# Kernel tuning notes

Hardware: AMD Instinct MI355X
Metric: run time of the kernel (lower is better)

Reference implementation:

```python
import jax, jax.numpy as jnp
import numpy as np

N = 10000          # nodes
DEG = 16           # incoming edges per node
E = N * DEG
D_IN = 2048        # backbone embed dim
RED = 4
D = D_IN // RED    # 512, gnn embed dim
NHEAD = 8
HD = D // NHEAD    # 64
DHID = 4 * D       # 2048, mlp hidden
L = 2              # num gnn layers
NCLS = 751
EPS = 1e-5


def _layernorm(x, g, b):
    m = jnp.mean(x, axis=-1, keepdims=True)
    v = jnp.var(x, axis=-1, keepdims=True)
    return (x - m) * jax.lax.rsqrt(v + EPS) * g + b


def _attention_layer(feats, r, c, Wq, bq, Wk, bk, Wv, bv, Wo, bo,
                     g1, be1, W1, b1, W2, b2, g2, be2):
    # MultiHeadDotProduct (dropout = identity in eval, mult_attr=0)
    q = (feats @ Wq.T + bq).reshape(N, NHEAD, HD)
    k = (feats @ Wk.T + bk).reshape(N, NHEAD, HD)
    v = (feats @ Wv.T + bv).reshape(N, NHEAD, HD)
    # per-edge scores: q gathered at target c, k gathered at source r
    scores = jnp.einsum('ehd,ehd->eh', q[c], k[r]) / np.float32(np.sqrt(HD))  # [E,H]
    # segment softmax grouped by target node c
    mx = jax.ops.segment_max(scores, c, num_segments=N)          # [N,H]
    ex = jnp.exp(scores - mx[c])
    den = jax.ops.segment_sum(ex, c, num_segments=N)             # [N,H]
    alpha = ex / den[c]                                          # [E,H]
    # weighted scatter-add of source values (aggr='add')
    agg = jax.ops.segment_sum(alpha[:, :, None] * v[r], c, num_segments=N)  # [N,H,HD]
    f2 = agg.reshape(N, D) @ Wo.T + bo
    # DotAttentionLayer: res1 + norm1 + mlp + res2 + norm2
    feats = _layernorm(feats + f2, g1, be1)
    f2 = jax.nn.relu(feats @ W1.T + b1) @ W2.T + b2
    return _layernorm(feats + f2, g2, be2)


def setup_inputs() -> dict:
    key = jax.random.key(0)
    ks = jax.random.split(key, 24)
    feats = jax.random.normal(ks[0], (N, D_IN), jnp.float32)
    # edge list: each target node c has DEG incoming edges from random sources r
    c = jnp.repeat(jnp.arange(N, dtype=jnp.int64), DEG)
    r = jax.random.randint(ks[1], (E,), 0, N, dtype=jnp.int64)
    edge_index = jnp.stack([r, c], axis=1)                       # [E,2]
    edge_attr = jax.random.uniform(ks[2], (E, 1), jnp.float32)
    s = 0.02
    inp = {
        'feats': feats, 'edge_index': edge_index, 'edge_attr': edge_attr,
        'Wred': jax.random.normal(ks[3], (D, D_IN), jnp.float32) * s,
        'bred': jnp.zeros((D,), jnp.float32),
        'Wq': jax.random.normal(ks[4], (L, D, D), jnp.float32) * s,
        'bq': jnp.zeros((L, D), jnp.float32),
        'Wk': jax.random.normal(ks[5], (L, D, D), jnp.float32) * s,
        'bk': jnp.zeros((L, D), jnp.float32),
        'Wv': jax.random.normal(ks[6], (L, D, D), jnp.float32) * s,
        'bv': jnp.zeros((L, D), jnp.float32),
        'Wo': jax.random.normal(ks[7], (L, D, D), jnp.float32) * s,
        'bo': jnp.zeros((L, D), jnp.float32),
        'g1': jnp.ones((L, D), jnp.float32),
        'be1': jnp.zeros((L, D), jnp.float32),
        'W1': jax.random.normal(ks[8], (L, DHID, D), jnp.float32) * s,
        'b1': jnp.zeros((L, DHID), jnp.float32),
        'W2': jax.random.normal(ks[9], (L, D, DHID), jnp.float32) * s,
        'b2': jnp.zeros((L, D), jnp.float32),
        'g2': jnp.ones((L, D), jnp.float32),
        'be2': jnp.zeros((L, D), jnp.float32),
        'bn_g': jnp.ones((D,), jnp.float32),
        'bn_b': jnp.zeros((D,), jnp.float32),
        'Wfc': jax.random.normal(ks[10], (NCLS, D), jnp.float32) * s,
    }
    return inp


def reference(feats, edge_index, edge_attr, Wred, bred, Wq, bq, Wk, bk, Wv, bv,
              Wo, bo, g1, be1, W1, b1, W2, b2, g2, be2, bn_g, bn_b, Wfc):
    r, c = edge_index[:, 0], edge_index[:, 1]
    # dim_red
    x = feats @ Wred.T + bred                                    # [N,D]
    # GNNNetwork: stacked DotAttentionLayers (out list, last taken since cat=0, every=0)
    for i in range(L):
        x = _attention_layer(x, r, c, Wq[i], bq[i], Wk[i], bk[i], Wv[i], bv[i],
                             Wo[i], bo[i], g1[i], be1[i], W1[i], b1[i],
                             W2[i], b2[i], g2[i], be2[i])
    feats_out = x
    # neck=1: BatchNorm1d in eval (running_mean=0, running_var=1) then bias-free fc
    bn = (feats_out * jax.lax.rsqrt(jnp.float32(1.0 + EPS))) * bn_g + bn_b
    logits = bn @ Wfc.T                                          # [N,NCLS]
    return (logits, feats_out)
```

## Files before the change

### kernel.cpp

```cpp
#include <hip/hip_runtime.h>
#include <hip/hip_bf16.h>

#define MPAD   10112
#define NR     10000
#define DM     512
#define DH     2048
#define DIN    2048
#define NCLS   751

typedef __attribute__((ext_vector_type(8))) short bf16x8;
typedef __attribute__((ext_vector_type(4))) float f32x4;
typedef __attribute__((address_space(3))) void lds_t;
typedef const __attribute__((address_space(1))) void glb_t;

static __device__ __forceinline__ float bf2f(unsigned short s) {
    union { unsigned u; float f; } c; c.u = ((unsigned)s) << 16; return c.f;
}
static __device__ __forceinline__ unsigned short f2bf(float f) {
    __hip_bfloat16 h = __float2bfloat16(f);
    return __builtin_bit_cast(unsigned short, h);
}

__global__ __launch_bounds__(256) void cvt8(
    const float* s0, const float* s1, const float* s2, const float* s3,
    const float* s4, const float* s5, const float* s6, const float* s7,
    unsigned short* d0, unsigned short* d1, unsigned short* d2, unsigned short* d3,
    unsigned short* d4, unsigned short* d5, unsigned short* d6, unsigned short* d7,
    int n0, int n1, int n2, int n3, int n4, int n5, int n6, int n7)
{
    const float* s; unsigned short* d; int n;
    switch (blockIdx.y) {
        case 0: s = s0; d = d0; n = n0; break;
        case 1: s = s1; d = d1; n = n1; break;
        case 2: s = s2; d = d2; n = n2; break;
        case 3: s = s3; d = d3; n = n3; break;
        case 4: s = s4; d = d4; n = n4; break;
        case 5: s = s5; d = d5; n = n5; break;
        case 6: s = s6; d = d6; n = n6; break;
        default: s = s7; d = d7; n = n7; break;
    }
    const int idx = (blockIdx.x * 256 + threadIdx.x) * 8;
    if (idx >= n) return;
    float4 a = *(const float4*)(s + idx);
    float4 b = *(const float4*)(s + idx + 4);
    union { unsigned short us[8]; int4 v; } o;
    o.us[0] = f2bf(a.x); o.us[1] = f2bf(a.y); o.us[2] = f2bf(a.z); o.us[3] = f2bf(a.w);
    o.us[4] = f2bf(b.x); o.us[5] = f2bf(b.y); o.us[6] = f2bf(b.z); o.us[7] = f2bf(b.w);
    *(int4*)(d + idx) = o.v;
}

__global__ __launch_bounds__(256) void cvt_fc(
    const float* __restrict__ Wfc, const float* __restrict__ g,
    unsigned short* __restrict__ out)
{
    const int idx = (blockIdx.x * 256 + threadIdx.x) * 8;
    if (idx >= NCLS * DM) return;
    const float s = rsqrtf(1.f + 1e-5f);
    union { unsigned short us[8]; int4 v; } o;
    #pragma unroll
    for (int j = 0; j < 8; ++j)
        o.us[j] = f2bf(Wfc[idx + j] * s * g[(idx + j) & (DM - 1)]);
    *(int4*)(out + idx) = o.v;
}

__global__ __launch_bounds__(64) void bnfc_bias(
    const float* __restrict__ Wfc, const float* __restrict__ bnb,
    float* __restrict__ biasfc)
{
    const int c = blockIdx.x;
    const int lane = threadIdx.x;
    const float* wp = Wfc + (size_t)c * DM + lane * 8;
    const float* bp = bnb + lane * 8;
    float s = 0.f;
    #pragma unroll
    for (int j = 0; j < 8; ++j) s += wp[j] * bp[j];
    #pragma unroll
    for (int off = 32; off > 0; off >>= 1) s += __shfl_xor(s, off, 64);
    if (lane == 0) biasfc[c] = s;
}

__global__ __launch_bounds__(256) void catbias(
    const float* __restrict__ bq, const float* __restrict__ bk,
    const float* __restrict__ bv, float* __restrict__ bqkv)
{
    const int t = blockIdx.x * 256 + threadIdx.x;
    if (t >= 2 * 3 * DM) return;
    const int l = t / (3 * DM), j = t % (3 * DM);
    float v;
    if (j < DM)          v = bq[l * DM + j];
    else if (j < 2 * DM) v = bk[l * DM + j - DM];
    else                 v = bv[l * DM + j - 2 * DM];
    bqkv[t] = v;
}

__global__ __launch_bounds__(256) void pad_feats(
    const float* __restrict__ f, unsigned short* __restrict__ h)
{
    const size_t t = (size_t)blockIdx.x * 256 + threadIdx.x;
    const size_t idx = t * 8;
    const int row = (int)(idx / DIN);
    union { unsigned short us[8]; int4 v; } o;
    if (row < NR) {
        float4 a = *(const float4*)(f + idx);
        float4 b = *(const float4*)(f + idx + 4);
        o.us[0] = f2bf(a.x); o.us[1] = f2bf(a.y); o.us[2] = f2bf(a.z); o.us[3] = f2bf(a.w);
        o.us[4] = f2bf(b.x); o.us[5] = f2bf(b.y); o.us[6] = f2bf(b.z); o.us[7] = f2bf(b.w);
    } else {
        o.v = (int4){0, 0, 0, 0};
    }
    *(int4*)(h + idx) = o.v;
}

static __device__ __forceinline__ int xcd_swizzle(int nwg) {
    const int d0  = blockIdx.y * gridDim.x + blockIdx.x;
    const int xcd = d0 & 7, dd = d0 >> 3;
    const int qc  = nwg >> 3, rc = nwg & 7;
    return (xcd < rc ? xcd * (qc + 1) : rc * (qc + 1) + (xcd - rc) * qc) + dd;
}


template<int EPI, bool GUARD>
__global__ __launch_bounds__(256) void gemm_bt(
    const unsigned short* __restrict__ A,
    const unsigned short* __restrict__ B,
    const float* __restrict__ bias,
    float* __restrict__ outF,
    unsigned short* __restrict__ outH,
    int K, int Nw, int ldc, int Mreal, int Nreal)
{
    __shared__ short As[128 * 64];
    __shared__ short Bs[128 * 64];
    const int tid  = threadIdx.x;
    const int lane = tid & 63;
    const int w    = tid >> 6;
    const int wm   = w >> 1, wn = w & 1;

    const int wgid = xcd_swizzle(gridDim.x * gridDim.y);
    const int bm0 = (wgid / gridDim.x) * 128;
    const int bn0 = (wgid % gridDim.x) * 128;

    f32x4 acc[4][4];
    #pragma unroll
    for (int i = 0; i < 4; ++i)
        #pragma unroll
        for (int j = 0; j < 4; ++j) acc[i][j] = (f32x4){0.f, 0.f, 0.f, 0.f};

    const int srow = lane >> 3;
    const int sslot = ((lane & 7) ^ srow) * 8;
    const int fr   = lane & 15;
    const int fr7  = fr & 7;
    const int c16  = lane >> 4;
    const int nkt  = K >> 6;

    for (int kt = 0; kt < nkt; ++kt) {
        if (kt) __syncthreads();
        #pragma unroll
        for (int c = 0; c < 4; ++c) {
            const int rb = c * 32 + w * 8;
            const int r  = rb + srow;
            const unsigned short* sa = A + (size_t)(bm0 + r) * K + kt * 64 + sslot;
            __builtin_amdgcn_global_load_lds((glb_t*)sa, (lds_t*)&As[rb * 64], 16, 0, 0);
            int br = bn0 + r; if (br >= Nw) br = Nw - 1;
            const unsigned short* sb = B + (size_t)br * K + kt * 64 + sslot;
            __builtin_amdgcn_global_load_lds((glb_t*)sb, (lds_t*)&Bs[rb * 64], 16, 0, 0);
        }
        __syncthreads();
        #pragma unroll
        for (int kk = 0; kk < 64; kk += 32) {
            const int slot = (((kk >> 3) + c16) ^ fr7) * 8;
            bf16x8 av[4], bv[4];
            #pragma unroll
            for (int mi = 0; mi < 4; ++mi)
                av[mi] = *(const bf16x8*)&As[(wm * 64 + mi * 16 + fr) * 64 + slot];
            #pragma unroll
            for (int ni = 0; ni < 4; ++ni)
                bv[ni] = *(const bf16x8*)&Bs[(wn * 64 + ni * 16 + fr) * 64 + slot];
            #pragma unroll
            for (int mi = 0; mi < 4; ++mi)
                #pragma unroll
                for (int ni = 0; ni < 4; ++ni)
                    acc[mi][ni] = __builtin_amdgcn_mfma_f32_16x16x32_bf16(
                        av[mi], bv[ni], acc[mi][ni], 0, 0, 0);
        }
    }

    const int rg = (lane >> 4) * 4;
    #pragma unroll
    for (int mi = 0; mi < 4; ++mi) {
        #pragma unroll
        for (int ni = 0; ni < 4; ++ni) {
            const int col = bn0 + wn * 64 + ni * 16 + fr;
            const int bcol = col < Nw ? col : Nw - 1;
            const float bvv = (EPI == 4) ? 0.f : bias[bcol];
            const f32x4 v = acc[mi][ni];
            #pragma unroll
            for (int j = 0; j < 4; ++j) {
                const int row = bm0 + wm * 64 + mi * 16 + rg + j;
                float val = v[j] + bvv;
                if (EPI == 3) val = fmaxf(val, 0.f);
                if (GUARD && (row >= Mreal || col >= Nreal)) continue;
                const size_t idx = (size_t)row * ldc + col;
                if (EPI == 0 || EPI == 1 || EPI == 4) outF[idx] = val;
                if (EPI == 1 || EPI == 2 || EPI == 3) outH[idx] = f2bf(val);
            }
        }
    }
}

template<int EPI, bool GUARD>
__global__ __launch_bounds__(256) void gemm_bt64(
    const unsigned short* __restrict__ A,
    const unsigned short* __restrict__ B,
    const float* __restrict__ bias,
    float* __restrict__ outF,
    unsigned short* __restrict__ outH,
    int K, int Nw, int ldc, int Mreal, int Nreal)
{
    __shared__ short As[64 * 64];
    __shared__ short Bs[64 * 64];
    const int tid  = threadIdx.x;
    const int lane = tid & 63;
    const int w    = tid >> 6;
    const int wm   = w >> 1, wn = w & 1;

    const int wgid = xcd_swizzle(gridDim.x * gridDim.y);
    const int bm0 = (wgid / gridDim.x) * 64;
    const int bn0 = (wgid % gridDim.x) * 64;

    f32x4 acc[2][2];
    #pragma unroll
    for (int i = 0; i < 2; ++i)
        #pragma unroll
        for (int j = 0; j < 2; ++j) acc[i][j] = (f32x4){0.f, 0.f, 0.f, 0.f};

    const int srow = lane >> 3;
    const int sslot = ((lane & 7) ^ srow) * 8;
    const int fr   = lane & 15;
    const int fr7  = fr & 7;
    const int c16  = lane >> 4;
    const int nkt  = K >> 6;

    for (int kt = 0; kt < nkt; ++kt) {
        if (kt) __syncthreads();
        #pragma unroll
        for (int c = 0; c < 2; ++c) {
            const int rb = c * 32 + w * 8;
            const int r  = rb + srow;
            const unsigned short* sa = A + (size_t)(bm0 + r) * K + kt * 64 + sslot;
            __builtin_amdgcn_global_load_lds((glb_t*)sa, (lds_t*)&As[rb * 64], 16, 0, 0);
            int br = bn0 + r; if (br >= Nw) br = Nw - 1;
            const unsigned short* sb = B + (size_t)br * K + kt * 64 + sslot;
            __builtin_amdgcn_global_load_lds((glb_t*)sb, (lds_t*)&Bs[rb * 64], 16, 0, 0);
        }
        __syncthreads();
        #pragma unroll
        for (int kk = 0; kk < 64; kk += 32) {
            const int slot = (((kk >> 3) + c16) ^ fr7) * 8;
            bf16x8 av[2], bv[2];
            #pragma unroll
            for (int mi = 0; mi < 2; ++mi)
                av[mi] = *(const bf16x8*)&As[(wm * 32 + mi * 16 + fr) * 64 + slot];
            #pragma unroll
            for (int ni = 0; ni < 2; ++ni)
                bv[ni] = *(const bf16x8*)&Bs[(wn * 32 + ni * 16 + fr) * 64 + slot];
            #pragma unroll
            for (int mi = 0; mi < 2; ++mi)
                #pragma unroll
                for (int ni = 0; ni < 2; ++ni)
                    acc[mi][ni] = __builtin_amdgcn_mfma_f32_16x16x32_bf16(
                        av[mi], bv[ni], acc[mi][ni], 0, 0, 0);
        }
    }

    const int rg = (lane >> 4) * 4;
    #pragma unroll
    for (int mi = 0; mi < 2; ++mi) {
        #pragma unroll
        for (int ni = 0; ni < 2; ++ni) {
            const int col = bn0 + wn * 32 + ni * 16 + fr;
            const int bcol = col < Nw ? col : Nw - 1;
            const float bvv = (EPI == 4) ? 0.f : bias[bcol];
            const f32x4 v = acc[mi][ni];
            #pragma unroll
            for (int j = 0; j < 4; ++j) {
                const int row = bm0 + wm * 32 + mi * 16 + rg + j;
                float val = v[j] + bvv;
                if (EPI == 3) val = fmaxf(val, 0.f);
                if (GUARD && (row >= Mreal || col >= Nreal)) continue;
                const size_t idx = (size_t)row * ldc + col;
                if (EPI == 0 || EPI == 1 || EPI == 4) outF[idx] = val;
                if (EPI == 1 || EPI == 2 || EPI == 3) outH[idx] = f2bf(val);
            }
        }
    }
}

__global__ __launch_bounds__(256) void attn_kernel(
    const unsigned short* __restrict__ qkv,
    const int* __restrict__ ei,
    unsigned short* __restrict__ aggb)
{
    const int wid  = threadIdx.x >> 6;
    const int lane = threadIdx.x & 63;
    const int iout = blockIdx.x * 4 + wid;
    const int i    = iout < NR ? iout : NR - 1;
    const int stride = (ei[33] == 0) ? 4 : 2;

    __shared__ int   sr[4][16];
    __shared__ float ssc[4][16 * 8];
    __shared__ float sal[4][16 * 8];

    bf16x8 qv = *(const bf16x8*)(qkv + (size_t)i * 1536 + lane * 8);
    float qf[8];
    #pragma unroll
    for (int j = 0; j < 8; ++j) qf[j] = bf2f((unsigned short)qv[j]);

    if (lane < 16) sr[wid][lane] = ei[((size_t)i * 16 + lane) * stride];
    __syncthreads();

    const int hh = lane >> 3;
    #pragma unroll 4
    for (int e = 0; e < 16; ++e) {
        const int r = sr[wid][e];
        bf16x8 kv = *(const bf16x8*)(qkv + (size_t)r * 1536 + DM + lane * 8);
        float dot = 0.f;
        #pragma unroll
        for (int j = 0; j < 8; ++j) dot += qf[j] * bf2f((unsigned short)kv[j]);
        dot += __shfl_xor(dot, 1, 64);
        dot += __shfl_xor(dot, 2, 64);
        dot += __shfl_xor(dot, 4, 64);
        if ((lane & 7) == 0) ssc[wid][e * 8 + hh] = dot * 0.125f;
    }
    __syncthreads();
    if (lane < 8) {
        float mx = -1e30f;
        for (int e = 0; e < 16; ++e) mx = fmaxf(mx, ssc[wid][e * 8 + lane]);
        float den = 0.f, ex[16];
        for (int e = 0; e < 16; ++e) { ex[e] = expf(ssc[wid][e * 8 + lane] - mx); den += ex[e]; }
        const float inv = 1.f / den;
        for (int e = 0; e < 16; ++e) sal[wid][e * 8 + lane] = ex[e] * inv;
    }
    __syncthreads();
    float accv[8] = {0, 0, 0, 0, 0, 0, 0, 0};
    #pragma unroll 4
    for (int e = 0; e < 16; ++e) {
        const int r = sr[wid][e];
        const float al = sal[wid][e * 8 + hh];
        bf16x8 vv = *(const bf16x8*)(qkv + (size_t)r * 1536 + 2 * DM + lane * 8);
        #pragma unroll
        for (int j = 0; j < 8; ++j) accv[j] += al * bf2f((unsigned short)vv[j]);
    }
    union { unsigned short us[8]; int4 v4; } o;
    if (iout < NR) {
        #pragma unroll
        for (int j = 0; j < 8; ++j) o.us[j] = f2bf(accv[j]);
    } else {
        o.v4 = (int4){0, 0, 0, 0};
    }
    *(int4*)(aggb + (size_t)iout * DM + lane * 8) = o.v4;
}

__global__ __launch_bounds__(64) void ln_kernel(
    float* __restrict__ x, const unsigned short* __restrict__ f2,
    const float* __restrict__ g, const float* __restrict__ be,
    unsigned short* __restrict__ xb, float* __restrict__ outFeats)
{
    const int row = blockIdx.x;
    const int lane = threadIdx.x;
    float* xp = x + (size_t)row * DM + lane * 8;
    const unsigned short* fp = f2 + (size_t)row * DM + lane * 8;
    float v[8];
    float4 a0 = *(const float4*)xp;
    float4 a1 = *(const float4*)(xp + 4);
    bf16x8 fv = *(const bf16x8*)fp;
    v[0]=a0.x; v[1]=a0.y; v[2]=a0.z; v[3]=a0.w;
    v[4]=a1.x; v[5]=a1.y; v[6]=a1.z; v[7]=a1.w;
    #pragma unroll
    for (int j = 0; j < 8; ++j) v[j] += bf2f((unsigned short)fv[j]);
    float s = 0.f, s2 = 0.f;
    #pragma unroll
    for (int j = 0; j < 8; ++j) { s += v[j]; s2 += v[j] * v[j]; }
    #pragma unroll
    for (int off = 32; off > 0; off >>= 1) {
        s  += __shfl_xor(s, off, 64);
        s2 += __shfl_xor(s2, off, 64);
    }
    const float mean = s * (1.f / DM);
    const float var  = s2 * (1.f / DM) - mean * mean;
    const float rs   = rsqrtf(var + 1e-5f);
    float y[8];
    union { unsigned short us[8]; int4 v4; } o;
    #pragma unroll
    for (int j = 0; j < 8; ++j) {
        const int d = lane * 8 + j;
        y[j] = (v[j] - mean) * rs * g[d] + be[d];
        o.us[j] = f2bf(y[j]);
    }
    float4 w0 = {y[0], y[1], y[2], y[3]}, w1 = {y[4], y[5], y[6], y[7]};
    *(float4*)xp = w0; *(float4*)(xp + 4) = w1;
    *(int4*)(xb + (size_t)row * DM + lane * 8) = o.v4;
    if (outFeats != nullptr && row < NR) {
        float* op = outFeats + (size_t)row * DM + lane * 8;
        *(float4*)op = w0; *(float4*)(op + 4) = w1;
    }
}

extern "C" void kernel_launch(void* const* d_in, const int* in_sizes, int n_in,
                              void* d_out, int out_size, void* d_ws, size_t ws_size,
                              hipStream_t stream)
{
    const float* feats = (const float*)d_in[0];
    const int* ei = (const int*)d_in[1];
    const float* Wred = (const float*)d_in[3];
    const float* bred = (const float*)d_in[4];
    const float* Wq = (const float*)d_in[5];
    const float* bq = (const float*)d_in[6];
    const float* Wk = (const float*)d_in[7];
    const float* bk = (const float*)d_in[8];
    const float* Wv = (const float*)d_in[9];
    const float* bv = (const float*)d_in[10];
    const float* Wo = (const float*)d_in[11];
    const float* bo = (const float*)d_in[12];
    const float* g1 = (const float*)d_in[13];
    const float* be1 = (const float*)d_in[14];
    const float* W1 = (const float*)d_in[15];
    const float* b1 = (const float*)d_in[16];
    const float* W2 = (const float*)d_in[17];
    const float* b2 = (const float*)d_in[18];
    const float* g2 = (const float*)d_in[19];
    const float* be2 = (const float*)d_in[20];
    const float* bng = (const float*)d_in[21];
    const float* bnb = (const float*)d_in[22];
    const float* Wfc = (const float*)d_in[23];

    char* ws = (char*)d_ws;
    size_t off = 0;
    auto alloc = [&](size_t bytes) {
        void* p = ws + off; off += (bytes + 255) & ~(size_t)255; return p;
    };
    unsigned short* h    = (unsigned short*)alloc((size_t)MPAD * DIN * 2);
    unsigned short* xb   = (unsigned short*)alloc((size_t)MPAD * DM * 2);
    unsigned short* qkvb = (unsigned short*)alloc((size_t)MPAD * 3 * DM * 2);
    unsigned short* aggb = (unsigned short*)alloc((size_t)MPAD * DM * 2);
    unsigned short* tmpH = (unsigned short*)alloc((size_t)MPAD * DM * 2);
    float* x   = (float*)alloc((size_t)MPAD * DM * 4);
    unsigned short* wredB = (unsigned short*)alloc((size_t)DM * DIN * 2);
    unsigned short* wqkvB = (unsigned short*)alloc((size_t)2 * 3 * DM * DM * 2);
    unsigned short* woB   = (unsigned short*)alloc((size_t)2 * DM * DM * 2);
    unsigned short* w1B   = (unsigned short*)alloc((size_t)2 * DH * DM * 2);
    unsigned short* w2B   = (unsigned short*)alloc((size_t)2 * DM * DH * 2);
    unsigned short* wfcB  = (unsigned short*)alloc((size_t)NCLS * DM * 2);
    float* bqkv   = (float*)alloc((size_t)2 * 3 * DM * 4);
    float* biasfc = (float*)alloc((size_t)NCLS * 4);

    const int MT  = MPAD / 128;
    const int MT2 = MPAD / 64;
    const int QK  = DM * DM;

    float* out = (float*)d_out;

    cvt8<<<dim3(QK / 8 / 256, 8), 256, 0, stream>>>(
        Wq, Wk, Wv, Wq + QK, Wk + QK, Wv + QK, nullptr, nullptr,
        wqkvB, wqkvB + QK, wqkvB + 2 * QK, wqkvB + 3 * QK, wqkvB + 4 * QK, wqkvB + 5 * QK,
        nullptr, nullptr,
        QK, QK, QK, QK, QK, QK, 0, 0);
    cvt8<<<dim3(2 * DH * DM / 8 / 256, 8), 256, 0, stream>>>(
        Wred, Wo, W1, W2, nullptr, nullptr, nullptr, nullptr,
        wredB, woB, w1B, w2B, nullptr, nullptr, nullptr, nullptr,
        DM * DIN, 2 * DM * DM, 2 * DH * DM, 2 * DM * DH, 0, 0, 0, 0);
    cvt_fc<<<(NCLS * DM / 8 + 255) / 256, 256, 0, stream>>>(Wfc, bng, wfcB);
    bnfc_bias<<<NCLS, 64, 0, stream>>>(Wfc, bnb, biasfc);
    catbias<<<(2 * 3 * DM + 255) / 256, 256, 0, stream>>>(bq, bk, bv, bqkv);
    pad_feats<<<MPAD * DIN / 8 / 256, 256, 0, stream>>>(feats, h);

    gemm_bt64<1, false><<<dim3(DM / 64, MT2), 256, 0, stream>>>(
        h, wredB, bred, x, xb, DIN, DM, DM, MPAD, DM);

    for (int l = 0; l < 2; ++l) {
        const size_t bOff = (size_t)l * DM;
        gemm_bt<2, false><<<dim3(12, MT), 256, 0, stream>>>(
            xb, wqkvB + (size_t)l * 3 * QK, bqkv + (size_t)l * 3 * DM,
            nullptr, qkvb, DM, 3 * DM, 3 * DM, MPAD, 3 * DM);
        attn_kernel<<<MPAD / 4, 256, 0, stream>>>(qkvb, ei, aggb);
        gemm_bt64<2, false><<<dim3(DM / 64, MT2), 256, 0, stream>>>(
            aggb, woB + (size_t)l * QK, bo + bOff, nullptr, tmpH, DM, DM, DM, MPAD, DM);
        ln_kernel<<<MPAD, 64, 0, stream>>>(x, tmpH, g1 + bOff, be1 + bOff, xb, nullptr);
        gemm_bt<3, false><<<dim3(16, MT), 256, 0, stream>>>(
            xb, w1B + (size_t)l * DH * DM, b1 + (size_t)l * DH, nullptr, h, DM, DH, DH, MPAD, DH);
        gemm_bt64<2, false><<<dim3(DM / 64, MT2), 256, 0, stream>>>(
            h, w2B + (size_t)l * DM * DH, b2 + bOff, nullptr, tmpH, DH, DM, DM, MPAD, DM);
        ln_kernel<<<MPAD, 64, 0, stream>>>(x, tmpH, g2 + bOff, be2 + bOff, xb,
                                           (l == 1) ? out + (size_t)NR * NCLS : nullptr);
    }

    gemm_bt64<0, true><<<dim3((NCLS + 63) / 64, MT2), 256, 0, stream>>>(
        xb, wfcB, biasfc, out, nullptr, DM, NCLS, NCLS, NR, NCLS);

    (void)in_sizes; (void)n_in; (void)out_size; (void)ws_size;
}
```

Before: 438.5 us.

## Fuse preprocessing kernels into one launch and double-buffer gemm_bt64 LDS tiles

Replaces six small conversion and bias kernels with one block-partitioned prep kernel, which removes several launch gaps. Separately, gemm_bt64 now double-buffers its A and B LDS tiles and prefetches the next k-tile with manual vmcnt waits and raw barriers, so global loads overlap the MFMA work. LDS use per block doubles, which can lower occupancy, and the hand-written waitcnt logic depends on an exact count of outstanding loads.

```diff
diff --git a/kernel.cpp b/kernel.cpp
--- a/kernel.cpp
+++ b/kernel.cpp
@@ -7,6 +7,7 @@
 #define DH     2048
 #define DIN    2048
 #define NCLS   751
+#define QKC    262144
 
 typedef __attribute__((ext_vector_type(8))) short bf16x8;
 typedef __attribute__((ext_vector_type(4))) float f32x4;
@@ -21,26 +22,12 @@
     return __builtin_bit_cast(unsigned short, h);
 }
 
-__global__ __launch_bounds__(256) void cvt8(
-    const float* s0, const float* s1, const float* s2, const float* s3,
-    const float* s4, const float* s5, const float* s6, const float* s7,
-    unsigned short* d0, unsigned short* d1, unsigned short* d2, unsigned short* d3,
-    unsigned short* d4, unsigned short* d5, unsigned short* d6, unsigned short* d7,
-    int n0, int n1, int n2, int n3, int n4, int n5, int n6, int n7)
-{
-    const float* s; unsigned short* d; int n;
-    switch (blockIdx.y) {
-        case 0: s = s0; d = d0; n = n0; break;
-        case 1: s = s1; d = d1; n = n1; break;
-        case 2: s = s2; d = d2; n = n2; break;
-        case 3: s = s3; d = d3; n = n3; break;
-        case 4: s = s4; d = d4; n = n4; break;
-        case 5: s = s5; d = d5; n = n5; break;
-        case 6: s = s6; d = d6; n = n6; break;
-        default: s = s7; d = d7; n = n7; break;
-    }
-    const int idx = (blockIdx.x * 256 + threadIdx.x) * 8;
-    if (idx >= n) return;
+#define PREP_BLOCKS 14084
+
+static __device__ __forceinline__ void cvt_blk(
+    const float* __restrict__ s, unsigned short* __restrict__ d, int rb, int tid)
+{
+    const int idx = (rb * 256 + tid) * 8;
     float4 a = *(const float4*)(s + idx);
     float4 b = *(const float4*)(s + idx + 4);
     union { unsigned short us[8]; int4 v; } o;
@@ -49,66 +36,95 @@
     *(int4*)(d + idx) = o.v;
 }
 
-__global__ __launch_bounds__(256) void cvt_fc(
-    const float* __restrict__ Wfc, const float* __restrict__ g,
-    unsigned short* __restrict__ out)
-{
-    const int idx = (blockIdx.x * 256 + threadIdx.x) * 8;
-    if (idx >= NCLS * DM) return;
-    const float s = rsqrtf(1.f + 1e-5f);
-    union { unsigned short us[8]; int4 v; } o;
-    #pragma unroll
-    for (int j = 0; j < 8; ++j)
-        o.us[j] = f2bf(Wfc[idx + j] * s * g[(idx + j) & (DM - 1)]);
-    *(int4*)(out + idx) = o.v;
-}
-
-__global__ __launch_bounds__(64) void bnfc_bias(
-    const float* __restrict__ Wfc, const float* __restrict__ bnb,
-    float* __restrict__ biasfc)
-{
-    const int c = blockIdx.x;
-    const int lane = threadIdx.x;
-    const float* wp = Wfc + (size_t)c * DM + lane * 8;
-    const float* bp = bnb + lane * 8;
-    float s = 0.f;
-    #pragma unroll
-    for (int j = 0; j < 8; ++j) s += wp[j] * bp[j];
-    #pragma unroll
-    for (int off = 32; off > 0; off >>= 1) s += __shfl_xor(s, off, 64);
-    if (lane == 0) biasfc[c] = s;
-}
-
-__global__ __launch_bounds__(256) void catbias(
-    const float* __restrict__ bq, const float* __restrict__ bk,
-    const float* __restrict__ bv, float* __restrict__ bqkv)
-{
-    const int t = blockIdx.x * 256 + threadIdx.x;
-    if (t >= 2 * 3 * DM) return;
-    const int l = t / (3 * DM), j = t % (3 * DM);
-    float v;
-    if (j < DM)          v = bq[l * DM + j];
-    else if (j < 2 * DM) v = bk[l * DM + j - DM];
-    else                 v = bv[l * DM + j - 2 * DM];
-    bqkv[t] = v;
-}
-
-__global__ __launch_bounds__(256) void pad_feats(
-    const float* __restrict__ f, unsigned short* __restrict__ h)
-{
-    const size_t t = (size_t)blockIdx.x * 256 + threadIdx.x;
-    const size_t idx = t * 8;
-    const int row = (int)(idx / DIN);
-    union { unsigned short us[8]; int4 v; } o;
-    if (row < NR) {
-        float4 a = *(const float4*)(f + idx);
-        float4 b = *(const float4*)(f + idx + 4);
-        o.us[0] = f2bf(a.x); o.us[1] = f2bf(a.y); o.us[2] = f2bf(a.z); o.us[3] = f2bf(a.w);
-        o.us[4] = f2bf(b.x); o.us[5] = f2bf(b.y); o.us[6] = f2bf(b.z); o.us[7] = f2bf(b.w);
-    } else {
-        o.v = (int4){0, 0, 0, 0};
-    }
-    *(int4*)(h + idx) = o.v;
+__global__ __launch_bounds__(256) void prep(
+    const float* Wq, const float* Wk, const float* Wv,
+    const float* Wred, const float* Wo, const float* W1, const float* W2,
+    const float* Wfc, const float* bng, const float* bnb,
+    const float* bq, const float* bk, const float* bv,
+    const float* feats,
+    unsigned short* wqkvB, unsigned short* wredB, unsigned short* woB,
+    unsigned short* w1B, unsigned short* w2B, unsigned short* wfcB,
+    float* biasfc, float* bqkv, unsigned short* h)
+{
+    int b = blockIdx.x;
+    const int tid = threadIdx.x;
+    if (b < 768) {
+        const int slice = b >> 7, rb = b & 127;
+        const float* s;
+        switch (slice) {
+            case 0: s = Wq; break;        case 1: s = Wk; break;
+            case 2: s = Wv; break;        case 3: s = Wq + QKC; break;
+            case 4: s = Wk + QKC; break;  default: s = Wv + QKC; break;
+        }
+        cvt_blk(s, wqkvB + (size_t)slice * QKC, rb, tid);
+        return;
+    }
+    b -= 768;
+    if (b < 512)  { cvt_blk(Wred, wredB, b, tid); return; }
+    b -= 512;
+    if (b < 256)  { cvt_blk(Wo, woB, b, tid); return; }
+    b -= 256;
+    if (b < 1024) { cvt_blk(W1, w1B, b, tid); return; }
+    b -= 1024;
+    if (b < 1024) { cvt_blk(W2, w2B, b, tid); return; }
+    b -= 1024;
+    if (b < 188) {
+        const int idx = (b * 256 + tid) * 8;
+        if (idx < NCLS * DM) {
+            const float s = rsqrtf(1.f + 1e-5f);
+            union { unsigned short us[8]; int4 v; } o;
+            #pragma unroll
+            for (int j = 0; j < 8; ++j)
+                o.us[j] = f2bf(Wfc[idx + j] * s * bng[(idx + j) & (DM - 1)]);
+            *(int4*)(wfcB + idx) = o.v;
+        }
+        return;
+    }
+    b -= 188;
+    if (b < 12) {
+        const int t = b * 256 + tid;
+        if (t < 2 * 3 * DM) {
+            const int l = t / (3 * DM), j = t % (3 * DM);
+            float v;
+            if (j < DM)          v = bq[l * DM + j];
+            else if (j < 2 * DM) v = bk[l * DM + j - DM];
+            else                 v = bv[l * DM + j - 2 * DM];
+            bqkv[t] = v;
+        }
+        return;
+    }
+    b -= 12;
+    if (b < 188) {
+        const int row = b * 4 + (tid >> 6);
+        const int lane = tid & 63;
+        if (row < NCLS) {
+            const float* wp = Wfc + (size_t)row * DM + lane * 8;
+            const float* bp = bnb + lane * 8;
+            float s = 0.f;
+            #pragma unroll
+            for (int j = 0; j < 8; ++j) s += wp[j] * bp[j];
+            #pragma unroll
+            for (int off = 32; off > 0; off >>= 1) s += __shfl_xor(s, off, 64);
+            if (lane == 0) biasfc[row] = s;
+        }
+        return;
+    }
+    b -= 188;
+    {
+        const size_t t = (size_t)b * 256 + tid;
+        const size_t idx = t * 8;
+        const int row = (int)(idx / DIN);
+        union { unsigned short us[8]; int4 v; } o;
+        if (row < NR) {
+            float4 a = *(const float4*)(feats + idx);
+            float4 c = *(const float4*)(feats + idx + 4);
+            o.us[0] = f2bf(a.x); o.us[1] = f2bf(a.y); o.us[2] = f2bf(a.z); o.us[3] = f2bf(a.w);
+            o.us[4] = f2bf(c.x); o.us[5] = f2bf(c.y); o.us[6] = f2bf(c.z); o.us[7] = f2bf(c.w);
+        } else {
+            o.v = (int4){0, 0, 0, 0};
+        }
+        *(int4*)(h + idx) = o.v;
+    }
 }
 
 static __device__ __forceinline__ int xcd_swizzle(int nwg) {
@@ -216,8 +232,8 @@
     unsigned short* __restrict__ outH,
     int K, int Nw, int ldc, int Mreal, int Nreal)
 {
-    __shared__ short As[64 * 64];
-    __shared__ short Bs[64 * 64];
+    __shared__ short As[2][64 * 64];
+    __shared__ short Bs[2][64 * 64];
     const int tid  = threadIdx.x;
     const int lane = tid & 63;
     const int w    = tid >> 6;
@@ -240,29 +256,40 @@
     const int c16  = lane >> 4;
     const int nkt  = K >> 6;
 
-    for (int kt = 0; kt < nkt; ++kt) {
-        if (kt) __syncthreads();
+    auto stage = [&](int kt, int buf) {
         #pragma unroll
         for (int c = 0; c < 2; ++c) {
             const int rb = c * 32 + w * 8;
             const int r  = rb + srow;
             const unsigned short* sa = A + (size_t)(bm0 + r) * K + kt * 64 + sslot;
-            __builtin_amdgcn_global_load_lds((glb_t*)sa, (lds_t*)&As[rb * 64], 16, 0, 0);
+            __builtin_amdgcn_global_load_lds((glb_t*)sa, (lds_t*)&As[buf][rb * 64], 16, 0, 0);
             int br = bn0 + r; if (br >= Nw) br = Nw - 1;
             const unsigned short* sb = B + (size_t)br * K + kt * 64 + sslot;
-            __builtin_amdgcn_global_load_lds((glb_t*)sb, (lds_t*)&Bs[rb * 64], 16, 0, 0);
-        }
-        __syncthreads();
+            __builtin_amdgcn_global_load_lds((glb_t*)sb, (lds_t*)&Bs[buf][rb * 64], 16, 0, 0);
+        }
+    };
+
+    stage(0, 0);
+    for (int kt = 0; kt < nkt; ++kt) {
+        const int cur = kt & 1;
+        if (kt + 1 < nkt) {
+            stage(kt + 1, cur ^ 1);
+            asm volatile("s_waitcnt vmcnt(4)" ::: "memory");
+        } else {
+            asm volatile("s_waitcnt vmcnt(0)" ::: "memory");
+        }
+        __builtin_amdgcn_s_barrier();
+        __builtin_amdgcn_sched_barrier(0);
         #pragma unroll
         for (int kk = 0; kk < 64; kk += 32) {
             const int slot = (((kk >> 3) + c16) ^ fr7) * 8;
             bf16x8 av[2], bv[2];
             #pragma unroll
             for (int mi = 0; mi < 2; ++mi)
-                av[mi] = *(const bf16x8*)&As[(wm * 32 + mi * 16 + fr) * 64 + slot];
+                av[mi] = *(const bf16x8*)&As[cur][(wm * 32 + mi * 16 + fr) * 64 + slot];
             #pragma unroll
             for (int ni = 0; ni < 2; ++ni)
-                bv[ni] = *(const bf16x8*)&Bs[(wn * 32 + ni * 16 + fr) * 64 + slot];
+                bv[ni] = *(const bf16x8*)&Bs[cur][(wn * 32 + ni * 16 + fr) * 64 + slot];
             #pragma unroll
             for (int mi = 0; mi < 2; ++mi)
                 #pragma unroll
@@ -270,6 +297,9 @@
                     acc[mi][ni] = __builtin_amdgcn_mfma_f32_16x16x32_bf16(
                         av[mi], bv[ni], acc[mi][ni], 0, 0, 0);
         }
+        asm volatile("s_waitcnt lgkmcnt(0)" ::: "memory");
+        __builtin_amdgcn_sched_barrier(0);
+        __builtin_amdgcn_s_barrier();
     }
 
     const int rg = (lane >> 4) * 4;
@@ -455,23 +485,12 @@
 
     const int MT  = MPAD / 128;
     const int MT2 = MPAD / 64;
-    const int QK  = DM * DM;
 
     float* out = (float*)d_out;
 
-    cvt8<<<dim3(QK / 8 / 256, 8), 256, 0, stream>>>(
-        Wq, Wk, Wv, Wq + QK, Wk + QK, Wv + QK, nullptr, nullptr,
-        wqkvB, wqkvB + QK, wqkvB + 2 * QK, wqkvB + 3 * QK, wqkvB + 4 * QK, wqkvB + 5 * QK,
-        nullptr, nullptr,
-        QK, QK, QK, QK, QK, QK, 0, 0);
-    cvt8<<<dim3(2 * DH * DM / 8 / 256, 8), 256, 0, stream>>>(
-        Wred, Wo, W1, W2, nullptr, nullptr, nullptr, nullptr,
-        wredB, woB, w1B, w2B, nullptr, nullptr, nullptr, nullptr,
-        DM * DIN, 2 * DM * DM, 2 * DH * DM, 2 * DM * DH, 0, 0, 0, 0);
-    cvt_fc<<<(NCLS * DM / 8 + 255) / 256, 256, 0, stream>>>(Wfc, bng, wfcB);
-    bnfc_bias<<<NCLS, 64, 0, stream>>>(Wfc, bnb, biasfc);
-    catbias<<<(2 * 3 * DM + 255) / 256, 256, 0, stream>>>(bq, bk, bv, bqkv);
-    pad_feats<<<MPAD * DIN / 8 / 256, 256, 0, stream>>>(feats, h);
+    prep<<<PREP_BLOCKS, 256, 0, stream>>>(
+        Wq, Wk, Wv, Wred, Wo, W1, W2, Wfc, bng, bnb, bq, bk, bv, feats,
+        wqkvB, wredB, woB, w1B, w2B, wfcB, biasfc, bqkv, h);
 
     gemm_bt64<1, false><<<dim3(DM / 64, MT2), 256, 0, stream>>>(
         h, wredB, bred, x, xb, DIN, DM, DM, MPAD, DM);
@@ -479,11 +498,11 @@
     for (int l = 0; l < 2; ++l) {
         const size_t bOff = (size_t)l * DM;
         gemm_bt<2, false><<<dim3(12, MT), 256, 0, stream>>>(
-            xb, wqkvB + (size_t)l * 3 * QK, bqkv + (size_t)l * 3 * DM,
+            xb, wqkvB + (size_t)l * 3 * QKC, bqkv + (size_t)l * 3 * DM,
             nullptr, qkvb, DM, 3 * DM, 3 * DM, MPAD, 3 * DM);
         attn_kernel<<<MPAD / 4, 256, 0, stream>>>(qkvb, ei, aggb);
         gemm_bt64<2, false><<<dim3(DM / 64, MT2), 256, 0, stream>>>(
-            aggb, woB + (size_t)l * QK, bo + bOff, nullptr, tmpH, DM, DM, DM, MPAD, DM);
+            aggb, woB + (size_t)l * QKC, bo + bOff, nullptr, tmpH, DM, DM, DM, MPAD, DM);
         ln_kernel<<<MPAD, 64, 0, stream>>>(x, tmpH, g1 + bOff, be1 + bOff, xb, nullptr);
         gemm_bt<3, false><<<dim3(16, MT), 256, 0, stream>>>(
             xb, w1B + (size_t)l * DH * DM, b1 + (size_t)l * DH, nullptr, h, DM, DH, DH, MPAD, DH);
```

Measured after the change: 454.1 us. +3.6%, slower.
